# Kernel optimization log

Hardware: AMD Instinct MI355X
Metric: run time of the kernel (lower is better)

Reference implementation:

```python
import jax, jax.numpy as jnp
import numpy as np

CLIP = 50.0
EPS = 1e-8


def _attn_jacobian_agg(q, k, v, scale):
    """Aggregate attention Jacobian dO/dq summed over queries, plus attention outputs.

    q: (B, Q, d); k, v: (B, S, d).
    Per-query Jacobian: J_q = scale * sum_j p_j v_j (k_j - kbar)^T, kbar = sum_i p_i k_i.
    Returns (agg_jac: (B, d, d), outputs: (B, Q, d)).
    """
    scores = jnp.einsum('bqd,bsd->bqs', q, k) * scale
    p = jax.nn.softmax(scores, axis=-1)
    out = jnp.einsum('bqs,bsd->bqd', p, v)           # attention outputs O
    kbar = jnp.einsum('bqs,bsd->bqd', p, k)          # expected key per query
    # sum_j p_j v_j k_j^T  -> (B, Q, d, d)
    pvk = jnp.einsum('bqs,bsd,bse->bqde', p, v, k)
    jac = scale * (pvk - out[..., :, None] * kbar[..., None, :])
    return jac.sum(axis=1), out


def setup_inputs() -> dict:
    key = jax.random.key(0)
    ks = jax.random.split(key, 5)
    B, Q, S, M, D = 256, 16, 512, 8, 128
    return {
        'queries': jax.random.normal(ks[0], (B, Q, D), dtype=jnp.float32),
        'keys':    jax.random.normal(ks[1], (B, S, D), dtype=jnp.float32),
        'values':  jax.random.normal(ks[2], (B, S, D), dtype=jnp.float32),
        'k_cg':    jax.random.normal(ks[3], (B, M, D), dtype=jnp.float32),
        'v_cg':    jax.random.normal(ks[4], (B, M, D), dtype=jnp.float32),
    }


def reference(queries, keys, values, k_cg, v_cg):
    B, Q, d = queries.shape
    scale = d ** -0.5

    dense_jac, dense_out = _attn_jacobian_agg(queries, keys, values, scale)
    cg_jac, cg_out = _attn_jacobian_agg(queries, k_cg, v_cg, scale)

    # jacobian_clip_value = 50.0 (config default)
    dense_jac = jnp.clip(dense_jac, -CLIP, CLIP)
    cg_jac = jnp.clip(cg_jac, -CLIP, CLIP)

    df = dense_jac.reshape(B, -1)
    cf = cg_jac.reshape(B, -1)
    dn = jnp.linalg.norm(df, axis=-1)
    cn = jnp.linalg.norm(cf, axis=-1)
    cosine_sim = (df * cf).sum(axis=-1) / (dn * cn + EPS)
    force_direction_loss = 1.0 - cosine_sim

    # consistency: per-query output MSE, averaged over queries, scaled by 1/d_head
    out_diff = dense_out - cg_out
    per_query_mse = (out_diff ** 2).sum(axis=-1)          # (B, Q)
    consistency_loss = per_query_mse.sum(axis=-1) / Q / d  # (B,)

    # v4 loss: L = w_dir * L_force_cos + w_cons * L_consistency (defaults 1.0, 1.0)
    total = 1.0 * force_direction_loss + 1.0 * consistency_loss
    return total.mean()  # reduction='mean'
```

## Files before the change

kernel.cpp:

```cpp
#include <hip/hip_runtime.h>
#include <math.h>


namespace {
constexpr int Bn = 256, Qn = 16, Sn = 512, Mn = 8, Dn = 128;
constexpr int NT = 512;
constexpr float SCALE = 0.08838834764831845f;
constexpr float CLIPV = 50.0f;

constexpr int PB   = 0;
constexpr int KT   = 16640;
constexpr int VT   = 25344;
constexpr int VTW  = 34048;
constexpr int WOFF = 42752;
constexpr int QS   = 44800;
constexpr int SCb  = 49152;
constexpr int PCG  = 50176;
constexpr int WC   = 51264;
constexpr int RED  = 51328;
constexpr int LDSZ = 51456;

typedef __attribute__((ext_vector_type(8))) short bf16x8;
typedef __attribute__((ext_vector_type(4))) float f32x4;
#define MFMA16(a, b, c) __builtin_amdgcn_mfma_f32_16x16x32_bf16((a), (b), (c), 0, 0, 0)

__device__ inline unsigned short f2bf(float x) {
  unsigned int u = __builtin_bit_cast(unsigned int, x);
  u += 0x7fffu + ((u >> 16) & 1u);
  return (unsigned short)(u >> 16);
}
__device__ inline float bf2f(unsigned short h) {
  unsigned int u = ((unsigned int)h) << 16;
  return __builtin_bit_cast(float, u);
}
__device__ inline unsigned int pack2(float a, float b) {
  return (unsigned int)f2bf(a) | ((unsigned int)f2bf(b) << 16);
}
union Frag {
  bf16x8 v;
  unsigned int u[4];
  unsigned short h[8];
};
__device__ inline bf16x8 lds4x32(const char* p) {
  Frag f;
  f.u[0] = *(const unsigned int*)(p);
  f.u[1] = *(const unsigned int*)(p + 4);
  f.u[2] = *(const unsigned int*)(p + 8);
  f.u[3] = *(const unsigned int*)(p + 12);
  return f.v;
}

__device__ inline void c_kstep(const char* L, int r0, int c0, int l16, int quad,
                               f32x4 C0[4], f32x4 C1[4]) {
  bf16x8 A0 = lds4x32(L + VTW + (r0 + l16) * 68 + quad * 16);
  bf16x8 A1 = lds4x32(L + VTW + (r0 + 16 + l16) * 68 + quad * 16);
#pragma unroll
  for (int j = 0; j < 4; ++j) {
    bf16x8 Bj = lds4x32(L + KT + (c0 + 16 * j + l16) * 68 + quad * 16);
    C0[j] = MFMA16(A0, Bj, C0[j]);
    C1[j] = MFMA16(A1, Bj, C1[j]);
  }
}

__global__ void zero_kernel(float* out) {
  if (threadIdx.x == 0) out[0] = 0.0f;
}

__global__ __launch_bounds__(NT, 2) void fm_kernel(
    const float* __restrict__ Qg, const float* __restrict__ Kg,
    const float* __restrict__ Vg, const float* __restrict__ Kcg,
    const float* __restrict__ Vcg, float* __restrict__ out) {
  __shared__ __align__(16) char L[LDSZ];
  const int b = blockIdx.x;
  const int t = threadIdx.x;
  const int lane = t & 63, wave = t >> 6;
  const int quad = lane >> 4, l16 = lane & 15;

  const float* Qb = Qg + (size_t)b * Qn * Dn;
  const float* Kb = Kg + (size_t)b * Sn * Dn;
  const float* Vb = Vg + (size_t)b * Sn * Dn;
  const float* Kc = Kcg + (size_t)b * Mn * Dn;
  const float* Vc = Vcg + (size_t)b * Mn * Dn;

  {
    int row = t >> 5, c4 = t & 31;
    float4 qv = ((const float4*)Qb)[t];
    unsigned long long pk = (unsigned long long)pack2(qv.x * SCALE, qv.y * SCALE) |
                            ((unsigned long long)pack2(qv.z * SCALE, qv.w * SCALE) << 32);
    *(unsigned long long*)(L + QS + row * 272 + c4 * 8) = pk;
  }

  bf16x8 aq[4];
  const bool score_wave = (wave < 4);
  float4 pf[4];
#pragma unroll
  for (int i = 0; i < 4; ++i) pf[i] = ((const float4*)Kb)[t + NT * i];
  for (int st = 0; st < 8; ++st) {
    __syncthreads();
#pragma unroll
    for (int i = 0; i < 4; ++i) {
      int g = t + NT * i;
      int row = g >> 5, c4 = g & 31;
      unsigned long long pk = (unsigned long long)pack2(pf[i].x, pf[i].y) |
                              ((unsigned long long)pack2(pf[i].z, pf[i].w) << 32);
      *(unsigned long long*)(L + KT + row * 272 + c4 * 8) = pk;
    }
    __syncthreads();
    if (st < 7) {
      const float4* nxt = (const float4*)(Kb + (size_t)(st + 1) * 64 * Dn);
#pragma unroll
      for (int i = 0; i < 4; ++i) pf[i] = nxt[t + NT * i];
    }
    if (st == 0 && score_wave) {
#pragma unroll
      for (int kk = 0; kk < 4; ++kk)
        aq[kk] = *(const bf16x8*)(L + QS + l16 * 272 + kk * 64 + quad * 16);
    }
    if (score_wave) {
      f32x4 acc = {0.f, 0.f, 0.f, 0.f};
#pragma unroll
      for (int kk = 0; kk < 4; ++kk) {
        bf16x8 bk = *(const bf16x8*)(L + KT + (wave * 16 + l16) * 272 + kk * 64 + quad * 16);
        acc = MFMA16(aq[kk], bk, acc);
      }
      int s = st * 64 + wave * 16 + l16;
#pragma unroll
      for (int r = 0; r < 4; ++r)
        *(unsigned short*)(L + PB + (quad * 4 + r) * 1040 + s * 2) = f2bf(acc[r]);
    }
  }
  __syncthreads();

#pragma unroll
  for (int rr = 0; rr < 2; ++rr) {
    int q = wave * 2 + rr;
    char* rowp = L + PB + q * 1040;
    Frag f;
    f.v = *(const bf16x8*)(rowp + lane * 16);
    float x[8];
    float m = -1e30f;
#pragma unroll
    for (int j = 0; j < 8; ++j) { x[j] = bf2f(f.h[j]); m = fmaxf(m, x[j]); }
#pragma unroll
    for (int o = 32; o; o >>= 1) m = fmaxf(m, __shfl_xor(m, o));
    float ssum = 0.f;
#pragma unroll
    for (int j = 0; j < 8; ++j) { x[j] = __expf(x[j] - m); ssum += x[j]; }
#pragma unroll
    for (int o = 32; o; o >>= 1) ssum += __shfl_xor(ssum, o);
    float inv = 1.f / ssum;
    Frag g2;
#pragma unroll
    for (int j = 0; j < 8; ++j) g2.h[j] = f2bf(x[j] * inv);
    *(bf16x8*)(rowp + lane * 16) = g2.v;
  }
  __syncthreads();
  {
    float wsv = 0.f;
#pragma unroll
    for (int q = 0; q < Qn; ++q)
      wsv += bf2f(*(const unsigned short*)(L + PB + q * 1040 + t * 2));
    *(float*)(L + WOFF + t * 4) = wsv;
  }
  __syncthreads();

  f32x4 C0[4], C1[4];
  f32x4 outacc = {0.f, 0.f, 0.f, 0.f}, kbacc = {0.f, 0.f, 0.f, 0.f};
#pragma unroll
  for (int j = 0; j < 4; ++j) { C0[j] = (f32x4){0.f, 0.f, 0.f, 0.f}; C1[j] = (f32x4){0.f, 0.f, 0.f, 0.f}; }
  const int rp = wave & 3, ch = wave >> 2;
  const int r0 = rp * 32, c0 = ch * 64;
  const int dq = t & 31, s2 = t >> 5;

  float4 k0 = ((const float4*)(Kb + (size_t)(2 * s2) * Dn))[dq];
  float4 k1 = ((const float4*)(Kb + (size_t)(2 * s2 + 1) * Dn))[dq];
  float4 v0 = ((const float4*)(Vb + (size_t)(2 * s2) * Dn))[dq];
  float4 v1 = ((const float4*)(Vb + (size_t)(2 * s2 + 1) * Dn))[dq];

  for (int st = 0; st < 16; ++st) {
    __syncthreads();
    {
      float w0 = *(const float*)(L + WOFF + (st * 32 + 2 * s2) * 4);
      float w1 = *(const float*)(L + WOFF + (st * 32 + 2 * s2 + 1) * 4);
      float ka[4] = {k0.x, k0.y, k0.z, k0.w}, kb2[4] = {k1.x, k1.y, k1.z, k1.w};
      float va[4] = {v0.x, v0.y, v0.z, v0.w}, vb2[4] = {v1.x, v1.y, v1.z, v1.w};
#pragma unroll
      for (int j = 0; j < 4; ++j) {
        int d = dq * 4 + j;
        *(unsigned int*)(L + KT + d * 68 + s2 * 4) = pack2(ka[j], kb2[j]);
        *(unsigned int*)(L + VT + d * 68 + s2 * 4) = pack2(va[j], vb2[j]);
        *(unsigned int*)(L + VTW + d * 68 + s2 * 4) = pack2(w0 * va[j], w1 * vb2[j]);
      }
    }
    __syncthreads();
    if (st < 15) {
      int srow = (st + 1) * 32 + 2 * s2;
      k0 = ((const float4*)(Kb + (size_t)srow * Dn))[dq];
      k1 = ((const float4*)(Kb + (size_t)(srow + 1) * Dn))[dq];
      v0 = ((const float4*)(Vb + (size_t)srow * Dn))[dq];
      v1 = ((const float4*)(Vb + (size_t)(srow + 1) * Dn))[dq];
    }
    {
      bf16x8 pA = *(const bf16x8*)(L + PB + l16 * 1040 + (st * 32 + quad * 8) * 2);
      bf16x8 bV = lds4x32(L + VT + (wave * 16 + l16) * 68 + quad * 16);
      bf16x8 bK = lds4x32(L + KT + (wave * 16 + l16) * 68 + quad * 16);
      outacc = MFMA16(pA, bV, outacc);
      kbacc = MFMA16(pA, bK, kbacc);
    }
    c_kstep(L, r0, c0, l16, quad, C0, C1);
  }
  __syncthreads();

#pragma unroll
  for (int r = 0; r < 4; ++r) {
    int d = wave * 16 + l16, q = quad * 4 + r;
    *(unsigned short*)(L + VTW + d * 68 + q * 2) = f2bf(-outacc[r]);
    *(unsigned short*)(L + KT + d * 68 + q * 2) = f2bf(kbacc[r]);
  }
  {
    int d = t & 127, part = t >> 7;
#pragma unroll
    for (int z = 0; z < 2; ++z) {
      int s2z = 8 + part * 2 + z;
      *(unsigned int*)(L + KT + d * 68 + s2z * 4) = 0u;
      *(unsigned int*)(L + VTW + d * 68 + s2z * 4) = 0u;
    }
  }
  __syncthreads();
  c_kstep(L, r0, c0, l16, quad, C0, C1);
#pragma unroll
  for (int j = 0; j < 4; ++j)
#pragma unroll
    for (int r = 0; r < 4; ++r) {
      C0[j][r] = fminf(fmaxf(SCALE * C0[j][r], -CLIPV), CLIPV);
      C1[j][r] = fminf(fmaxf(SCALE * C1[j][r], -CLIPV), CLIPV);
    }

  __syncthreads();
  if (t < 256) {
    int row = t >> 5, c4 = t & 31;
    float4 kv = ((const float4*)Kc)[t];
    unsigned long long pk = (unsigned long long)pack2(kv.x, kv.y) |
                            ((unsigned long long)pack2(kv.z, kv.w) << 32);
    *(unsigned long long*)(L + KT + row * 272 + c4 * 8) = pk;
  }
  __syncthreads();
  if (wave == 0) {
    f32x4 acc = {0.f, 0.f, 0.f, 0.f};
#pragma unroll
    for (int kk = 0; kk < 4; ++kk) {
      bf16x8 a = *(const bf16x8*)(L + QS + l16 * 272 + kk * 64 + quad * 16);
      bf16x8 bk = *(const bf16x8*)(L + KT + (l16 & 7) * 272 + kk * 64 + quad * 16);
      acc = MFMA16(a, bk, acc);
    }
#pragma unroll
    for (int r = 0; r < 4; ++r)
      *(float*)(L + SCb + (quad * 4 + r) * 64 + l16 * 4) = acc[r];
  }
  __syncthreads();
  if (t < 16) {
    float xs[8];
    float m = -1e30f;
#pragma unroll
    for (int s = 0; s < 8; ++s) { xs[s] = *(const float*)(L + SCb + t * 64 + s * 4); m = fmaxf(m, xs[s]); }
    float ssum = 0.f;
#pragma unroll
    for (int s = 0; s < 8; ++s) { xs[s] = __expf(xs[s] - m); ssum += xs[s]; }
    float inv = 1.f / ssum;
#pragma unroll
    for (int s = 0; s < 8; ++s) *(unsigned short*)(L + PCG + t * 68 + s * 2) = f2bf(xs[s] * inv);
#pragma unroll
    for (int s = 8; s < 32; ++s) *(unsigned short*)(L + PCG + t * 68 + s * 2) = 0;
  }
  __syncthreads();
  if (t < 8) {
    float wsv = 0.f;
#pragma unroll
    for (int q = 0; q < 16; ++q)
      wsv += bf2f(*(const unsigned short*)(L + PCG + q * 68 + t * 2));
    *(float*)(L + WC + t * 4) = wsv;
  }
  __syncthreads();
  {
    int d = t & 127, grp = t >> 7;
    float kc0 = Kc[(size_t)(2 * grp) * Dn + d], kc1 = Kc[(size_t)(2 * grp + 1) * Dn + d];
    float vc0 = Vc[(size_t)(2 * grp) * Dn + d], vc1 = Vc[(size_t)(2 * grp + 1) * Dn + d];
    float wc0 = *(const float*)(L + WC + (2 * grp) * 4);
    float wc1 = *(const float*)(L + WC + (2 * grp + 1) * 4);
    *(unsigned int*)(L + KT + d * 68 + grp * 4) = pack2(kc0, kc1);
    *(unsigned int*)(L + VT + d * 68 + grp * 4) = pack2(vc0, vc1);
    *(unsigned int*)(L + VTW + d * 68 + grp * 4) = pack2(wc0 * vc0, wc1 * vc1);
#pragma unroll
    for (int z = 0; z < 3; ++z) {
      int s2z = 4 + grp * 3 + z;
      *(unsigned int*)(L + KT + d * 68 + s2z * 4) = 0u;
      *(unsigned int*)(L + VT + d * 68 + s2z * 4) = 0u;
      *(unsigned int*)(L + VTW + d * 68 + s2z * 4) = 0u;
    }
  }
  __syncthreads();
  f32x4 outc = {0.f, 0.f, 0.f, 0.f}, kbc = {0.f, 0.f, 0.f, 0.f};
  {
    bf16x8 pA = lds4x32(L + PCG + l16 * 68 + quad * 16);
    bf16x8 bV = lds4x32(L + VT + (wave * 16 + l16) * 68 + quad * 16);
    bf16x8 bK = lds4x32(L + KT + (wave * 16 + l16) * 68 + quad * 16);
    outc = MFMA16(pA, bV, outc);
    kbc = MFMA16(pA, bK, kbc);
  }
  f32x4 D0[4], D1[4];
#pragma unroll
  for (int j = 0; j < 4; ++j) { D0[j] = (f32x4){0.f, 0.f, 0.f, 0.f}; D1[j] = (f32x4){0.f, 0.f, 0.f, 0.f}; }
  c_kstep(L, r0, c0, l16, quad, D0, D1);
  __syncthreads();
#pragma unroll
  for (int r = 0; r < 4; ++r) {
    int d = wave * 16 + l16, q = quad * 4 + r;
    *(unsigned short*)(L + VTW + d * 68 + q * 2) = f2bf(-outc[r]);
    *(unsigned short*)(L + KT + d * 68 + q * 2) = f2bf(kbc[r]);
  }
  {
    int d = t & 127, part = t >> 7;
#pragma unroll
    for (int z = 0; z < 2; ++z) {
      int s2z = 8 + part * 2 + z;
      *(unsigned int*)(L + KT + d * 68 + s2z * 4) = 0u;
      *(unsigned int*)(L + VTW + d * 68 + s2z * 4) = 0u;
    }
  }
  __syncthreads();
  c_kstep(L, r0, c0, l16, quad, D0, D1);
#pragma unroll
  for (int j = 0; j < 4; ++j)
#pragma unroll
    for (int r = 0; r < 4; ++r) {
      D0[j][r] = fminf(fmaxf(SCALE * D0[j][r], -CLIPV), CLIPV);
      D1[j][r] = fminf(fmaxf(SCALE * D1[j][r], -CLIPV), CLIPV);
    }

  float dot = 0.f, nd2 = 0.f, nc2 = 0.f, cons = 0.f;
#pragma unroll
  for (int j = 0; j < 4; ++j)
#pragma unroll
    for (int r = 0; r < 4; ++r) {
      dot += C0[j][r] * D0[j][r] + C1[j][r] * D1[j][r];
      nd2 += C0[j][r] * C0[j][r] + C1[j][r] * C1[j][r];
      nc2 += D0[j][r] * D0[j][r] + D1[j][r] * D1[j][r];
    }
#pragma unroll
  for (int r = 0; r < 4; ++r) {
    float df = outacc[r] - outc[r];
    cons += df * df;
  }
#pragma unroll
  for (int o = 32; o; o >>= 1) {
    dot += __shfl_xor(dot, o);
    nd2 += __shfl_xor(nd2, o);
    nc2 += __shfl_xor(nc2, o);
    cons += __shfl_xor(cons, o);
  }
  if (lane == 0) {
    float* red = (float*)(L + RED);
    red[wave * 4 + 0] = dot;
    red[wave * 4 + 1] = nd2;
    red[wave * 4 + 2] = nc2;
    red[wave * 4 + 3] = cons;
  }
  __syncthreads();
  if (t == 0) {
    const float* red = (const float*)(L + RED);
    float d_ = 0.f, n1 = 0.f, n2 = 0.f, cs = 0.f;
#pragma unroll
    for (int w = 0; w < 8; ++w) {
      d_ += red[w * 4 + 0];
      n1 += red[w * 4 + 1];
      n2 += red[w * 4 + 2];
      cs += red[w * 4 + 3];
    }
    float cosv = d_ / (sqrtf(n1) * sqrtf(n2) + 1e-8f);
    float lb = (1.0f - cosv) + cs / (float)(Qn * Dn);
    atomicAdd(out, lb * (1.0f / (float)Bn));
  }
}
}

extern "C" void kernel_launch(void* const* d_in, const int* in_sizes, int n_in,
                              void* d_out, int out_size, void* d_ws, size_t ws_size,
                              hipStream_t stream) {
  const float* q = (const float*)d_in[0];
  const float* k = (const float*)d_in[1];
  const float* v = (const float*)d_in[2];
  const float* kc = (const float*)d_in[3];
  const float* vc = (const float*)d_in[4];
  float* out = (float*)d_out;
  zero_kernel<<<1, 64, 0, stream>>>(out);
  fm_kernel<<<Bn, NT, 0, stream>>>(q, k, v, kc, vc, out);
}
```

Measured before the change: 171.2 us.

## Split each batch across two blocks by V-column half with workspace reduction

Each batch element is now handled by two blocks, one per half of the value dimension. Each block computes a 64x128 slice of the Jacobian, and the partial dot/norm/consistency sums are combined through a global workspace and a finalize kernel. The change also reads scores directly from global K instead of staging K through LDS, and stores K/V tiles in a wider 64-sequence transposed LDS layout with 16-byte accesses. The bf16 pack now truncates via a byte permute instead of rounding. This doubles the grid for better CU occupancy, at the cost of duplicated score/softmax work and K loads per block, an extra kernel launch, and some precision loss from truncation.

After: 169.0 us. Within noise of the previous version (-1.3%).

```diff
diff --git a/kernel.cpp b/kernel.cpp
--- a/kernel.cpp
+++ b/kernel.cpp
@@ -8,22 +8,28 @@
 constexpr float SCALE = 0.08838834764831845f;
 constexpr float CLIPV = 50.0f;
 
-constexpr int PB   = 0;
-constexpr int KT   = 16640;
-constexpr int VT   = 25344;
-constexpr int VTW  = 34048;
-constexpr int WOFF = 42752;
-constexpr int QS   = 44800;
-constexpr int SCb  = 49152;
-constexpr int PCG  = 50176;
-constexpr int WC   = 51264;
-constexpr int RED  = 51328;
-constexpr int LDSZ = 51456;
+constexpr int QS    = 0;
+constexpr int PB    = 4352;
+constexpr int WOFF  = 20992;
+constexpr int ARENA = 23040;
+constexpr int KT    = ARENA;
+constexpr int VT    = ARENA + 18432;
+constexpr int VTW   = ARENA + 27648;
+constexpr int SCF   = ARENA;
+constexpr int CGS   = 59904;
+constexpr int PCG   = 60416;
+constexpr int WC    = 61696;
+constexpr int RED   = 61728;
+constexpr int LDSZ  = 61856;
 
 typedef __attribute__((ext_vector_type(8))) short bf16x8;
 typedef __attribute__((ext_vector_type(4))) float f32x4;
 #define MFMA16(a, b, c) __builtin_amdgcn_mfma_f32_16x16x32_bf16((a), (b), (c), 0, 0, 0)
 
+__device__ inline unsigned int pack2t(float a, float b) {
+  return __builtin_amdgcn_perm(__builtin_bit_cast(unsigned int, b),
+                               __builtin_bit_cast(unsigned int, a), 0x07060302u);
+}
 __device__ inline unsigned short f2bf(float x) {
   unsigned int u = __builtin_bit_cast(unsigned int, x);
   u += 0x7fffu + ((u >> 16) & 1u);
@@ -32,48 +38,38 @@
 __device__ inline float bf2f(unsigned short h) {
   unsigned int u = ((unsigned int)h) << 16;
   return __builtin_bit_cast(float, u);
-}
-__device__ inline unsigned int pack2(float a, float b) {
-  return (unsigned int)f2bf(a) | ((unsigned int)f2bf(b) << 16);
 }
 union Frag {
   bf16x8 v;
   unsigned int u[4];
   unsigned short h[8];
 };
-__device__ inline bf16x8 lds4x32(const char* p) {
-  Frag f;
-  f.u[0] = *(const unsigned int*)(p);
-  f.u[1] = *(const unsigned int*)(p + 4);
-  f.u[2] = *(const unsigned int*)(p + 8);
-  f.u[3] = *(const unsigned int*)(p + 12);
-  return f.v;
-}
-
-__device__ inline void c_kstep(const char* L, int r0, int c0, int l16, int quad,
-                               f32x4 C0[4], f32x4 C1[4]) {
-  bf16x8 A0 = lds4x32(L + VTW + (r0 + l16) * 68 + quad * 16);
-  bf16x8 A1 = lds4x32(L + VTW + (r0 + 16 + l16) * 68 + quad * 16);
-#pragma unroll
-  for (int j = 0; j < 4; ++j) {
-    bf16x8 Bj = lds4x32(L + KT + (c0 + 16 * j + l16) * 68 + quad * 16);
-    C0[j] = MFMA16(A0, Bj, C0[j]);
-    C1[j] = MFMA16(A1, Bj, C1[j]);
-  }
-}
-
-__global__ void zero_kernel(float* out) {
-  if (threadIdx.x == 0) out[0] = 0.0f;
-}
-
-__global__ __launch_bounds__(NT, 2) void fm_kernel(
+
+__global__ void zero_ws_kernel(float4* ws) {
+  ws[threadIdx.x] = make_float4(0.f, 0.f, 0.f, 0.f);
+}
+
+__global__ void finalize_kernel(const float* __restrict__ ws, float* __restrict__ out) {
+  __shared__ float sr[256];
+  int i = threadIdx.x;
+  float dt = ws[i * 4 + 0], n1 = ws[i * 4 + 1], n2 = ws[i * 4 + 2], cs = ws[i * 4 + 3];
+  float cosv = dt / (sqrtf(n1) * sqrtf(n2) + 1e-8f);
+  sr[i] = (1.0f - cosv) + cs * (1.0f / (float)(Qn * Dn));
+  __syncthreads();
+  for (int off = 128; off; off >>= 1) {
+    if (i < off) sr[i] += sr[i + off];
+    __syncthreads();
+  }
+  if (i == 0) out[0] = sr[0] * (1.0f / (float)Bn);
+}
+
+__global__ __launch_bounds__(NT, 4) void fm_kernel(
     const float* __restrict__ Qg, const float* __restrict__ Kg,
     const float* __restrict__ Vg, const float* __restrict__ Kcg,
-    const float* __restrict__ Vcg, float* __restrict__ out) {
+    const float* __restrict__ Vcg, float* __restrict__ ws) {
   __shared__ __align__(16) char L[LDSZ];
-  const int b = blockIdx.x;
-  const int t = threadIdx.x;
-  const int lane = t & 63, wave = t >> 6;
+  const int bid = blockIdx.x, b = bid >> 1, h = bid & 1;
+  const int t = threadIdx.x, lane = t & 63, wv = t >> 6;
   const int quad = lane >> 4, l16 = lane & 15;
 
   const float* Qb = Qg + (size_t)b * Qn * Dn;
@@ -82,77 +78,101 @@
   const float* Kc = Kcg + (size_t)b * Mn * Dn;
   const float* Vc = Vcg + (size_t)b * Mn * Dn;
 
+  const int dK = t & 127, gK = t >> 7;
+  const int dV = t & 63, gV = t >> 6;
+  float kpf[2][8], vpf[8];
+
+  auto load_tiles = [&](int st) {
+#pragma unroll
+    for (int o = 0; o < 2; ++o) {
+      int s0 = st * 64 + (gK + 4 * o) * 8;
+#pragma unroll
+      for (int i = 0; i < 8; ++i) kpf[o][i] = Kb[(size_t)(s0 + i) * Dn + dK];
+    }
+    int s1 = st * 64 + gV * 8;
+#pragma unroll
+    for (int i = 0; i < 8; ++i) vpf[i] = Vb[(size_t)(s1 + i) * Dn + h * 64 + dV];
+  };
+  auto store_tiles = [&](int st) {
+#pragma unroll
+    for (int o = 0; o < 2; ++o) {
+      unsigned int u0 = pack2t(kpf[o][0], kpf[o][1]), u1 = pack2t(kpf[o][2], kpf[o][3]);
+      unsigned int u2 = pack2t(kpf[o][4], kpf[o][5]), u3 = pack2t(kpf[o][6], kpf[o][7]);
+      *(uint4*)(L + KT + dK * 144 + (gK + 4 * o) * 16) = make_uint4(u0, u1, u2, u3);
+    }
+    int s1 = st * 64 + gV * 8;
+    float wv8[8];
+#pragma unroll
+    for (int i = 0; i < 8; ++i) wv8[i] = *(const float*)(L + WOFF + (s1 + i) * 4);
+    unsigned int v0 = pack2t(vpf[0], vpf[1]), v1 = pack2t(vpf[2], vpf[3]);
+    unsigned int v2 = pack2t(vpf[4], vpf[5]), v3 = pack2t(vpf[6], vpf[7]);
+    *(uint4*)(L + VT + dV * 144 + gV * 16) = make_uint4(v0, v1, v2, v3);
+    unsigned int w0 = pack2t(wv8[0] * vpf[0], wv8[1] * vpf[1]);
+    unsigned int w1 = pack2t(wv8[2] * vpf[2], wv8[3] * vpf[3]);
+    unsigned int w2 = pack2t(wv8[4] * vpf[4], wv8[5] * vpf[5]);
+    unsigned int w3 = pack2t(wv8[6] * vpf[6], wv8[7] * vpf[7]);
+    *(uint4*)(L + VTW + dV * 144 + gV * 16) = make_uint4(w0, w1, w2, w3);
+  };
+
   {
     int row = t >> 5, c4 = t & 31;
     float4 qv = ((const float4*)Qb)[t];
-    unsigned long long pk = (unsigned long long)pack2(qv.x * SCALE, qv.y * SCALE) |
-                            ((unsigned long long)pack2(qv.z * SCALE, qv.w * SCALE) << 32);
-    *(unsigned long long*)(L + QS + row * 272 + c4 * 8) = pk;
-  }
-
-  bf16x8 aq[4];
-  const bool score_wave = (wave < 4);
-  float4 pf[4];
-#pragma unroll
-  for (int i = 0; i < 4; ++i) pf[i] = ((const float4*)Kb)[t + NT * i];
-  for (int st = 0; st < 8; ++st) {
-    __syncthreads();
-#pragma unroll
-    for (int i = 0; i < 4; ++i) {
-      int g = t + NT * i;
-      int row = g >> 5, c4 = g & 31;
-      unsigned long long pk = (unsigned long long)pack2(pf[i].x, pf[i].y) |
-                              ((unsigned long long)pack2(pf[i].z, pf[i].w) << 32);
-      *(unsigned long long*)(L + KT + row * 272 + c4 * 8) = pk;
-    }
-    __syncthreads();
-    if (st < 7) {
-      const float4* nxt = (const float4*)(Kb + (size_t)(st + 1) * 64 * Dn);
-#pragma unroll
-      for (int i = 0; i < 4; ++i) pf[i] = nxt[t + NT * i];
-    }
-    if (st == 0 && score_wave) {
-#pragma unroll
-      for (int kk = 0; kk < 4; ++kk)
-        aq[kk] = *(const bf16x8*)(L + QS + l16 * 272 + kk * 64 + quad * 16);
-    }
-    if (score_wave) {
+    unsigned int p0 = pack2t(qv.x * SCALE, qv.y * SCALE);
+    unsigned int p1 = pack2t(qv.z * SCALE, qv.w * SCALE);
+    *(unsigned long long*)(L + QS + row * 272 + c4 * 8) =
+        (unsigned long long)p0 | ((unsigned long long)p1 << 32);
+  }
+  load_tiles(0);
+  __syncthreads();
+
+  {
+    bf16x8 aq[4];
+#pragma unroll
+    for (int kk = 0; kk < 4; ++kk)
+      aq[kk] = *(const bf16x8*)(L + QS + l16 * 272 + kk * 64 + quad * 16);
+    for (int j = 0; j < 4; ++j) {
+      int srow = 64 * wv + 16 * j + l16;
+      const float* kp = Kb + (size_t)srow * Dn + quad * 8;
       f32x4 acc = {0.f, 0.f, 0.f, 0.f};
 #pragma unroll
       for (int kk = 0; kk < 4; ++kk) {
-        bf16x8 bk = *(const bf16x8*)(L + KT + (wave * 16 + l16) * 272 + kk * 64 + quad * 16);
-        acc = MFMA16(aq[kk], bk, acc);
+        float4 lo = *(const float4*)(kp + kk * 32);
+        float4 hi = *(const float4*)(kp + kk * 32 + 4);
+        Frag f;
+        f.u[0] = pack2t(lo.x, lo.y);
+        f.u[1] = pack2t(lo.z, lo.w);
+        f.u[2] = pack2t(hi.x, hi.y);
+        f.u[3] = pack2t(hi.z, hi.w);
+        acc = MFMA16(aq[kk], f.v, acc);
       }
-      int s = st * 64 + wave * 16 + l16;
+      int s = 64 * wv + 16 * j + l16;
 #pragma unroll
       for (int r = 0; r < 4; ++r)
-        *(unsigned short*)(L + PB + (quad * 4 + r) * 1040 + s * 2) = f2bf(acc[r]);
+        *(float*)(L + SCF + (quad * 4 + r) * 2064 + s * 4) = acc[r];
     }
   }
   __syncthreads();
 
 #pragma unroll
   for (int rr = 0; rr < 2; ++rr) {
-    int q = wave * 2 + rr;
-    char* rowp = L + PB + q * 1040;
-    Frag f;
-    f.v = *(const bf16x8*)(rowp + lane * 16);
+    int q = wv * 2 + rr;
+    const float* srow = (const float*)(L + SCF + q * 2064);
     float x[8];
     float m = -1e30f;
 #pragma unroll
-    for (int j = 0; j < 8; ++j) { x[j] = bf2f(f.h[j]); m = fmaxf(m, x[j]); }
+    for (int i = 0; i < 8; ++i) { x[i] = srow[lane * 8 + i]; m = fmaxf(m, x[i]); }
 #pragma unroll
     for (int o = 32; o; o >>= 1) m = fmaxf(m, __shfl_xor(m, o));
     float ssum = 0.f;
 #pragma unroll
-    for (int j = 0; j < 8; ++j) { x[j] = __expf(x[j] - m); ssum += x[j]; }
+    for (int i = 0; i < 8; ++i) { x[i] = __expf(x[i] - m); ssum += x[i]; }
 #pragma unroll
     for (int o = 32; o; o >>= 1) ssum += __shfl_xor(ssum, o);
     float inv = 1.f / ssum;
-    Frag g2;
-#pragma unroll
-    for (int j = 0; j < 8; ++j) g2.h[j] = f2bf(x[j] * inv);
-    *(bf16x8*)(rowp + lane * 16) = g2.v;
+    Frag g;
+#pragma unroll
+    for (int i = 0; i < 8; ++i) g.h[i] = f2bf(x[i] * inv);
+    *(bf16x8*)(L + PB + q * 1040 + lane * 16) = g.v;
   }
   __syncthreads();
   {
@@ -164,192 +184,192 @@
   }
   __syncthreads();
 
-  f32x4 C0[4], C1[4];
-  f32x4 outacc = {0.f, 0.f, 0.f, 0.f}, kbacc = {0.f, 0.f, 0.f, 0.f};
-#pragma unroll
-  for (int j = 0; j < 4; ++j) { C0[j] = (f32x4){0.f, 0.f, 0.f, 0.f}; C1[j] = (f32x4){0.f, 0.f, 0.f, 0.f}; }
-  const int rp = wave & 3, ch = wave >> 2;
-  const int r0 = rp * 32, c0 = ch * 64;
-  const int dq = t & 31, s2 = t >> 5;
-
-  float4 k0 = ((const float4*)(Kb + (size_t)(2 * s2) * Dn))[dq];
-  float4 k1 = ((const float4*)(Kb + (size_t)(2 * s2 + 1) * Dn))[dq];
-  float4 v0 = ((const float4*)(Vb + (size_t)(2 * s2) * Dn))[dq];
-  float4 v1 = ((const float4*)(Vb + (size_t)(2 * s2 + 1) * Dn))[dq];
-
-  for (int st = 0; st < 16; ++st) {
+  const int rp = wv & 1, ch = wv >> 1;
+  f32x4 C00 = {0.f,0.f,0.f,0.f}, C01 = {0.f,0.f,0.f,0.f};
+  f32x4 C10 = {0.f,0.f,0.f,0.f}, C11 = {0.f,0.f,0.f,0.f};
+  f32x4 outacc = {0.f,0.f,0.f,0.f}, kbacc = {0.f,0.f,0.f,0.f};
+
+  auto ckstep = [&](int colByte, f32x4& c00, f32x4& c01, f32x4& c10, f32x4& c11) {
+    bf16x8 A0 = *(const bf16x8*)(L + VTW + (rp * 32 + l16) * 144 + colByte + quad * 16);
+    bf16x8 A1 = *(const bf16x8*)(L + VTW + (rp * 32 + 16 + l16) * 144 + colByte + quad * 16);
+    bf16x8 B0 = *(const bf16x8*)(L + KT + (ch * 32 + l16) * 144 + colByte + quad * 16);
+    bf16x8 B1 = *(const bf16x8*)(L + KT + (ch * 32 + 16 + l16) * 144 + colByte + quad * 16);
+    c00 = MFMA16(A0, B0, c00);
+    c01 = MFMA16(A0, B1, c01);
+    c10 = MFMA16(A1, B0, c10);
+    c11 = MFMA16(A1, B1, c11);
+  };
+
+  for (int st = 0; st < 8; ++st) {
+    if (st) __syncthreads();
+    store_tiles(st);
     __syncthreads();
-    {
-      float w0 = *(const float*)(L + WOFF + (st * 32 + 2 * s2) * 4);
-      float w1 = *(const float*)(L + WOFF + (st * 32 + 2 * s2 + 1) * 4);
-      float ka[4] = {k0.x, k0.y, k0.z, k0.w}, kb2[4] = {k1.x, k1.y, k1.z, k1.w};
-      float va[4] = {v0.x, v0.y, v0.z, v0.w}, vb2[4] = {v1.x, v1.y, v1.z, v1.w};
-#pragma unroll
-      for (int j = 0; j < 4; ++j) {
-        int d = dq * 4 + j;
-        *(unsigned int*)(L + KT + d * 68 + s2 * 4) = pack2(ka[j], kb2[j]);
-        *(unsigned int*)(L + VT + d * 68 + s2 * 4) = pack2(va[j], vb2[j]);
-        *(unsigned int*)(L + VTW + d * 68 + s2 * 4) = pack2(w0 * va[j], w1 * vb2[j]);
+    if (st < 7) load_tiles(st + 1);
+#pragma unroll
+    for (int z = 0; z < 2; ++z) {
+      int colByte = z * 64;
+      bf16x8 pA = *(const bf16x8*)(L + PB + l16 * 1040 + st * 128 + z * 64 + quad * 16);
+      bf16x8 bK = *(const bf16x8*)(L + KT + (wv * 16 + l16) * 144 + colByte + quad * 16);
+      kbacc = MFMA16(pA, bK, kbacc);
+      if (wv < 4) {
+        bf16x8 bV = *(const bf16x8*)(L + VT + (wv * 16 + l16) * 144 + colByte + quad * 16);
+        outacc = MFMA16(pA, bV, outacc);
       }
-    }
-    __syncthreads();
-    if (st < 15) {
-      int srow = (st + 1) * 32 + 2 * s2;
-      k0 = ((const float4*)(Kb + (size_t)srow * Dn))[dq];
-      k1 = ((const float4*)(Kb + (size_t)(srow + 1) * Dn))[dq];
-      v0 = ((const float4*)(Vb + (size_t)srow * Dn))[dq];
-      v1 = ((const float4*)(Vb + (size_t)(srow + 1) * Dn))[dq];
-    }
-    {
-      bf16x8 pA = *(const bf16x8*)(L + PB + l16 * 1040 + (st * 32 + quad * 8) * 2);
-      bf16x8 bV = lds4x32(L + VT + (wave * 16 + l16) * 68 + quad * 16);
-      bf16x8 bK = lds4x32(L + KT + (wave * 16 + l16) * 68 + quad * 16);
-      outacc = MFMA16(pA, bV, outacc);
-      kbacc = MFMA16(pA, bK, kbacc);
-    }
-    c_kstep(L, r0, c0, l16, quad, C0, C1);
-  }
-  __syncthreads();
-
+      ckstep(colByte, C00, C01, C10, C11);
+    }
+  }
+  __syncthreads();
+
+  if (wv < 4) {
+#pragma unroll
+    for (int r = 0; r < 4; ++r)
+      *(unsigned short*)(L + VTW + (wv * 16 + l16) * 144 + (quad * 4 + r) * 2) = f2bf(-outacc[r]);
+  }
+#pragma unroll
+  for (int r = 0; r < 4; ++r)
+    *(unsigned short*)(L + KT + (wv * 16 + l16) * 144 + (quad * 4 + r) * 2) = f2bf(kbacc[r]);
+  if (t < 256) {
+    *(uint4*)(L + KT + (t >> 1) * 144 + 32 + (t & 1) * 16) = make_uint4(0, 0, 0, 0);
+  } else if (t < 384) {
+    int i = t - 256;
+    *(uint4*)(L + VTW + (i >> 1) * 144 + 32 + (i & 1) * 16) = make_uint4(0, 0, 0, 0);
+  }
+  __syncthreads();
+  ckstep(0, C00, C01, C10, C11);
 #pragma unroll
   for (int r = 0; r < 4; ++r) {
-    int d = wave * 16 + l16, q = quad * 4 + r;
-    *(unsigned short*)(L + VTW + d * 68 + q * 2) = f2bf(-outacc[r]);
-    *(unsigned short*)(L + KT + d * 68 + q * 2) = f2bf(kbacc[r]);
-  }
-  {
-    int d = t & 127, part = t >> 7;
-#pragma unroll
-    for (int z = 0; z < 2; ++z) {
-      int s2z = 8 + part * 2 + z;
-      *(unsigned int*)(L + KT + d * 68 + s2z * 4) = 0u;
-      *(unsigned int*)(L + VTW + d * 68 + s2z * 4) = 0u;
-    }
-  }
-  __syncthreads();
-  c_kstep(L, r0, c0, l16, quad, C0, C1);
-#pragma unroll
-  for (int j = 0; j < 4; ++j)
-#pragma unroll
-    for (int r = 0; r < 4; ++r) {
-      C0[j][r] = fminf(fmaxf(SCALE * C0[j][r], -CLIPV), CLIPV);
-      C1[j][r] = fminf(fmaxf(SCALE * C1[j][r], -CLIPV), CLIPV);
-    }
-
-  __syncthreads();
-  if (t < 256) {
-    int row = t >> 5, c4 = t & 31;
-    float4 kv = ((const float4*)Kc)[t];
-    unsigned long long pk = (unsigned long long)pack2(kv.x, kv.y) |
-                            ((unsigned long long)pack2(kv.z, kv.w) << 32);
-    *(unsigned long long*)(L + KT + row * 272 + c4 * 8) = pk;
-  }
-  __syncthreads();
-  if (wave == 0) {
+    C00[r] = fminf(fmaxf(SCALE * C00[r], -CLIPV), CLIPV);
+    C01[r] = fminf(fmaxf(SCALE * C01[r], -CLIPV), CLIPV);
+    C10[r] = fminf(fmaxf(SCALE * C10[r], -CLIPV), CLIPV);
+    C11[r] = fminf(fmaxf(SCALE * C11[r], -CLIPV), CLIPV);
+  }
+  __syncthreads();
+
+  if (wv == 0) {
     f32x4 acc = {0.f, 0.f, 0.f, 0.f};
+    const float* kp = Kc + (size_t)(l16 & 7) * Dn + quad * 8;
 #pragma unroll
     for (int kk = 0; kk < 4; ++kk) {
       bf16x8 a = *(const bf16x8*)(L + QS + l16 * 272 + kk * 64 + quad * 16);
-      bf16x8 bk = *(const bf16x8*)(L + KT + (l16 & 7) * 272 + kk * 64 + quad * 16);
-      acc = MFMA16(a, bk, acc);
-    }
-#pragma unroll
-    for (int r = 0; r < 4; ++r)
-      *(float*)(L + SCb + (quad * 4 + r) * 64 + l16 * 4) = acc[r];
+      float4 lo = *(const float4*)(kp + kk * 32);
+      float4 hi = *(const float4*)(kp + kk * 32 + 4);
+      Frag f;
+      f.u[0] = pack2t(lo.x, lo.y);
+      f.u[1] = pack2t(lo.z, lo.w);
+      f.u[2] = pack2t(hi.x, hi.y);
+      f.u[3] = pack2t(hi.z, hi.w);
+      acc = MFMA16(a, f.v, acc);
+    }
+    if (l16 < 8) {
+#pragma unroll
+      for (int r = 0; r < 4; ++r)
+        *(float*)(L + CGS + (quad * 4 + r) * 32 + l16 * 4) = acc[r];
+    }
   }
   __syncthreads();
   if (t < 16) {
     float xs[8];
     float m = -1e30f;
 #pragma unroll
-    for (int s = 0; s < 8; ++s) { xs[s] = *(const float*)(L + SCb + t * 64 + s * 4); m = fmaxf(m, xs[s]); }
+    for (int s = 0; s < 8; ++s) { xs[s] = *(const float*)(L + CGS + t * 32 + s * 4); m = fmaxf(m, xs[s]); }
     float ssum = 0.f;
 #pragma unroll
     for (int s = 0; s < 8; ++s) { xs[s] = __expf(xs[s] - m); ssum += xs[s]; }
     float inv = 1.f / ssum;
 #pragma unroll
-    for (int s = 0; s < 8; ++s) *(unsigned short*)(L + PCG + t * 68 + s * 2) = f2bf(xs[s] * inv);
-#pragma unroll
-    for (int s = 8; s < 32; ++s) *(unsigned short*)(L + PCG + t * 68 + s * 2) = 0;
+    for (int s = 0; s < 4; ++s)
+      *(unsigned int*)(L + PCG + t * 80 + s * 4) = pack2t(xs[2 * s] * inv, xs[2 * s + 1] * inv);
+#pragma unroll
+    for (int p = 4; p < 16; ++p) *(unsigned int*)(L + PCG + t * 80 + p * 4) = 0u;
   }
   __syncthreads();
   if (t < 8) {
-    float wsv = 0.f;
-#pragma unroll
-    for (int q = 0; q < 16; ++q)
-      wsv += bf2f(*(const unsigned short*)(L + PCG + q * 68 + t * 2));
-    *(float*)(L + WC + t * 4) = wsv;
-  }
-  __syncthreads();
+    float s = 0.f;
+#pragma unroll
+    for (int q = 0; q < Qn; ++q) s += bf2f(*(const unsigned short*)(L + PCG + q * 80 + t * 2));
+    *(float*)(L + WC + t * 4) = s;
+  }
+  __syncthreads();
+  if (t < 128) {
+    float kv[8];
+#pragma unroll
+    for (int i = 0; i < 8; ++i) kv[i] = Kc[(size_t)i * Dn + t];
+    *(uint4*)(L + KT + t * 144) = make_uint4(pack2t(kv[0], kv[1]), pack2t(kv[2], kv[3]),
+                                             pack2t(kv[4], kv[5]), pack2t(kv[6], kv[7]));
+    *(uint4*)(L + KT + t * 144 + 16) = make_uint4(0, 0, 0, 0);
+    *(uint4*)(L + KT + t * 144 + 32) = make_uint4(0, 0, 0, 0);
+    *(uint4*)(L + KT + t * 144 + 48) = make_uint4(0, 0, 0, 0);
+  } else if (t < 192) {
+    int d = t - 128;
+    float vv2[8];
+#pragma unroll
+    for (int i = 0; i < 8; ++i) vv2[i] = Vc[(size_t)i * Dn + h * 64 + d];
+    *(uint4*)(L + VT + d * 144) = make_uint4(pack2t(vv2[0], vv2[1]), pack2t(vv2[2], vv2[3]),
+                                             pack2t(vv2[4], vv2[5]), pack2t(vv2[6], vv2[7]));
+    *(uint4*)(L + VT + d * 144 + 16) = make_uint4(0, 0, 0, 0);
+    *(uint4*)(L + VT + d * 144 + 32) = make_uint4(0, 0, 0, 0);
+    *(uint4*)(L + VT + d * 144 + 48) = make_uint4(0, 0, 0, 0);
+  } else if (t < 256) {
+    int d = t - 192;
+    float vv2[8], wcv[8];
+#pragma unroll
+    for (int i = 0; i < 8; ++i) {
+      vv2[i] = Vc[(size_t)i * Dn + h * 64 + d];
+      wcv[i] = *(const float*)(L + WC + i * 4);
+    }
+    *(uint4*)(L + VTW + d * 144) =
+        make_uint4(pack2t(wcv[0] * vv2[0], wcv[1] * vv2[1]), pack2t(wcv[2] * vv2[2], wcv[3] * vv2[3]),
+                   pack2t(wcv[4] * vv2[4], wcv[5] * vv2[5]), pack2t(wcv[6] * vv2[6], wcv[7] * vv2[7]));
+    *(uint4*)(L + VTW + d * 144 + 16) = make_uint4(0, 0, 0, 0);
+    *(uint4*)(L + VTW + d * 144 + 32) = make_uint4(0, 0, 0, 0);
+    *(uint4*)(L + VTW + d * 144 + 48) = make_uint4(0, 0, 0, 0);
+  }
+  __syncthreads();
+  f32x4 outc = {0.f,0.f,0.f,0.f}, kbc = {0.f,0.f,0.f,0.f};
+  f32x4 D00 = {0.f,0.f,0.f,0.f}, D01 = {0.f,0.f,0.f,0.f};
+  f32x4 D10 = {0.f,0.f,0.f,0.f}, D11 = {0.f,0.f,0.f,0.f};
   {
-    int d = t & 127, grp = t >> 7;
-    float kc0 = Kc[(size_t)(2 * grp) * Dn + d], kc1 = Kc[(size_t)(2 * grp + 1) * Dn + d];
-    float vc0 = Vc[(size_t)(2 * grp) * Dn + d], vc1 = Vc[(size_t)(2 * grp + 1) * Dn + d];
-    float wc0 = *(const float*)(L + WC + (2 * grp) * 4);
-    float wc1 = *(const float*)(L + WC + (2 * grp + 1) * 4);
-    *(unsigned int*)(L + KT + d * 68 + grp * 4) = pack2(kc0, kc1);
-    *(unsigned int*)(L + VT + d * 68 + grp * 4) = pack2(vc0, vc1);
-    *(unsigned int*)(L + VTW + d * 68 + grp * 4) = pack2(wc0 * vc0, wc1 * vc1);
-#pragma unroll
-    for (int z = 0; z < 3; ++z) {
-      int s2z = 4 + grp * 3 + z;
-      *(unsigned int*)(L + KT + d * 68 + s2z * 4) = 0u;
-      *(unsigned int*)(L + VT + d * 68 + s2z * 4) = 0u;
-      *(unsigned int*)(L + VTW + d * 68 + s2z * 4) = 0u;
-    }
-  }
-  __syncthreads();
-  f32x4 outc = {0.f, 0.f, 0.f, 0.f}, kbc = {0.f, 0.f, 0.f, 0.f};
-  {
-    bf16x8 pA = lds4x32(L + PCG + l16 * 68 + quad * 16);
-    bf16x8 bV = lds4x32(L + VT + (wave * 16 + l16) * 68 + quad * 16);
-    bf16x8 bK = lds4x32(L + KT + (wave * 16 + l16) * 68 + quad * 16);
-    outc = MFMA16(pA, bV, outc);
+    bf16x8 pA = *(const bf16x8*)(L + PCG + l16 * 80 + quad * 16);
+    bf16x8 bK = *(const bf16x8*)(L + KT + (wv * 16 + l16) * 144 + quad * 16);
     kbc = MFMA16(pA, bK, kbc);
-  }
-  f32x4 D0[4], D1[4];
-#pragma unroll
-  for (int j = 0; j < 4; ++j) { D0[j] = (f32x4){0.f, 0.f, 0.f, 0.f}; D1[j] = (f32x4){0.f, 0.f, 0.f, 0.f}; }
-  c_kstep(L, r0, c0, l16, quad, D0, D1);
-  __syncthreads();
+    if (wv < 4) {
+      bf16x8 bV = *(const bf16x8*)(L + VT + (wv * 16 + l16) * 144 + quad * 16);
+      outc = MFMA16(pA, bV, outc);
+    }
+    ckstep(0, D00, D01, D10, D11);
+  }
+  __syncthreads();
+  if (wv < 4) {
+#pragma unroll
+    for (int r = 0; r < 4; ++r)
+      *(unsigned short*)(L + VTW + (wv * 16 + l16) * 144 + (quad * 4 + r) * 2) = f2bf(-outc[r]);
+  }
+#pragma unroll
+  for (int r = 0; r < 4; ++r)
+    *(unsigned short*)(L + KT + (wv * 16 + l16) * 144 + (quad * 4 + r) * 2) = f2bf(kbc[r]);
+  __syncthreads();
+  ckstep(0, D00, D01, D10, D11);
 #pragma unroll
   for (int r = 0; r < 4; ++r) {
-    int d = wave * 16 + l16, q = quad * 4 + r;
-    *(unsigned short*)(L + VTW + d * 68 + q * 2) = f2bf(-outc[r]);
-    *(unsigned short*)(L + KT + d * 68 + q * 2) = f2bf(kbc[r]);
-  }
-  {
-    int d = t & 127, part = t >> 7;
-#pragma unroll
-    for (int z = 0; z < 2; ++z) {
-      int s2z = 8 + part * 2 + z;
-      *(unsigned int*)(L + KT + d * 68 + s2z * 4) = 0u;
-      *(unsigned int*)(L + VTW + d * 68 + s2z * 4) = 0u;
-    }
-  }
-  __syncthreads();
-  c_kstep(L, r0, c0, l16, quad, D0, D1);
-#pragma unroll
-  for (int j = 0; j < 4; ++j)
+    D00[r] = fminf(fmaxf(SCALE * D00[r], -CLIPV), CLIPV);
+    D01[r] = fminf(fmaxf(SCALE * D01[r], -CLIPV), CLIPV);
+    D10[r] = fminf(fmaxf(SCALE * D10[r], -CLIPV), CLIPV);
+    D11[r] = fminf(fmaxf(SCALE * D11[r], -CLIPV), CLIPV);
+  }
+
+  float dot = 0.f, nd2 = 0.f, nc2 = 0.f, cons = 0.f;
+#pragma unroll
+  for (int r = 0; r < 4; ++r) {
+    dot += C00[r] * D00[r] + C01[r] * D01[r] + C10[r] * D10[r] + C11[r] * D11[r];
+    nd2 += C00[r] * C00[r] + C01[r] * C01[r] + C10[r] * C10[r] + C11[r] * C11[r];
+    nc2 += D00[r] * D00[r] + D01[r] * D01[r] + D10[r] * D10[r] + D11[r] * D11[r];
+  }
+  if (wv < 4) {
 #pragma unroll
     for (int r = 0; r < 4; ++r) {
-      D0[j][r] = fminf(fmaxf(SCALE * D0[j][r], -CLIPV), CLIPV);
-      D1[j][r] = fminf(fmaxf(SCALE * D1[j][r], -CLIPV), CLIPV);
-    }
-
-  float dot = 0.f, nd2 = 0.f, nc2 = 0.f, cons = 0.f;
-#pragma unroll
-  for (int j = 0; j < 4; ++j)
-#pragma unroll
-    for (int r = 0; r < 4; ++r) {
-      dot += C0[j][r] * D0[j][r] + C1[j][r] * D1[j][r];
-      nd2 += C0[j][r] * C0[j][r] + C1[j][r] * C1[j][r];
-      nc2 += D0[j][r] * D0[j][r] + D1[j][r] * D1[j][r];
-    }
-#pragma unroll
-  for (int r = 0; r < 4; ++r) {
-    float df = outacc[r] - outc[r];
-    cons += df * df;
+      float df = outacc[r] - outc[r];
+      cons += df * df;
+    }
   }
 #pragma unroll
   for (int o = 32; o; o >>= 1) {
@@ -360,10 +380,10 @@
   }
   if (lane == 0) {
     float* red = (float*)(L + RED);
-    red[wave * 4 + 0] = dot;
-    red[wave * 4 + 1] = nd2;
-    red[wave * 4 + 2] = nc2;
-    red[wave * 4 + 3] = cons;
+    red[wv * 4 + 0] = dot;
+    red[wv * 4 + 1] = nd2;
+    red[wv * 4 + 2] = nc2;
+    red[wv * 4 + 3] = cons;
   }
   __syncthreads();
   if (t == 0) {
@@ -376,9 +396,10 @@
       n2 += red[w * 4 + 2];
       cs += red[w * 4 + 3];
     }
-    float cosv = d_ / (sqrtf(n1) * sqrtf(n2) + 1e-8f);
-    float lb = (1.0f - cosv) + cs / (float)(Qn * Dn);
-    atomicAdd(out, lb * (1.0f / (float)Bn));
+    atomicAdd(ws + b * 4 + 0, d_);
+    atomicAdd(ws + b * 4 + 1, n1);
+    atomicAdd(ws + b * 4 + 2, n2);
+    atomicAdd(ws + b * 4 + 3, cs);
   }
 }
 }
@@ -392,6 +413,8 @@
   const float* kc = (const float*)d_in[3];
   const float* vc = (const float*)d_in[4];
   float* out = (float*)d_out;
-  zero_kernel<<<1, 64, 0, stream>>>(out);
-  fm_kernel<<<Bn, NT, 0, stream>>>(q, k, v, kc, vc, out);
-}
+  float* ws = (float*)d_ws;
+  zero_ws_kernel<<<1, 256, 0, stream>>>((float4*)ws);
+  fm_kernel<<<2 * Bn, NT, 0, stream>>>(q, k, v, kc, vc, ws);
+  finalize_kernel<<<1, 256, 0, stream>>>(ws, out);
+}
```
